# Performance work log

Measured on AMD Instinct MI355X. Metric: run time of the kernel, lower is better.

## Reference

```python
import jax, jax.numpy as jnp
import numpy as np

N_NODES = 100000


def _graph_conv_right(feat, src, dst, W, b, n_nodes):
    # DGL GraphConv(norm='right'): since in_feats > out_feats, apply weight first,
    # then sum-aggregate messages over edges, divide by in-degree (clamped >= 1),
    # add bias, then relu activation.
    h = feat @ W                                   # [N, out]
    msg = jnp.take(h, src, axis=0)                 # [E, out] gather from source nodes
    agg = jax.ops.segment_sum(msg, dst, num_segments=n_nodes)  # [N, out]
    deg = jax.ops.segment_sum(jnp.ones_like(dst, dtype=feat.dtype), dst,
                              num_segments=n_nodes)
    deg = jnp.clip(deg, 1.0, None)                 # allow_zero_in_degree
    out = agg / deg[:, None] + b
    return jax.nn.relu(out)


def setup_inputs() -> dict:
    key = jax.random.key(0)
    ks = jax.random.split(key, 6)
    n_edges = 3200000
    in_dim, hidden_dim, out_dim = 128, 32, 12
    features = jax.random.normal(ks[0], (N_NODES, in_dim), dtype=jnp.float32)
    src = jax.random.randint(ks[1], (n_edges,), 0, N_NODES, dtype=jnp.int64 if jax.config.jax_enable_x64 else jnp.int32)
    dst = jax.random.randint(ks[2], (n_edges,), 0, N_NODES, dtype=jnp.int64 if jax.config.jax_enable_x64 else jnp.int32)
    W1 = jax.random.normal(ks[3], (in_dim, hidden_dim), dtype=jnp.float32) * (1.0 / np.sqrt(in_dim))
    b1 = jnp.zeros((hidden_dim,), dtype=jnp.float32)
    W2 = jax.random.normal(ks[4], (hidden_dim, out_dim), dtype=jnp.float32) * (1.0 / np.sqrt(hidden_dim))
    b2 = jnp.zeros((out_dim,), dtype=jnp.float32)
    return {"features": features, "src": src, "dst": dst,
            "W1": W1, "b1": b1, "W2": W2, "b2": b2}


def reference(features, src, dst, W1, b1, W2, b2):
    x = _graph_conv_right(features, src, dst, W1, b1, N_NODES)
    x = jax.nn.relu(x)  # extra F.relu after layer1 (idempotent, kept for fidelity)
    x = _graph_conv_right(x, src, dst, W2, b2, N_NODES)
    return x
```

## Files before the change

kernel.cpp:

```cpp
#include <hip/hip_runtime.h>
#include <hip/hip_fp16.h>

#define N_IN   128
#define HID    32
#define ODIM   12
#define H2P    16
#define RNODES 128
#define NBMAX  800
#define NBK2   1024
#define BCAP   4608
#define CHUNK  8192

__global__ __launch_bounds__(256) void gemm1_kernel(const float* __restrict__ feat,
                                                    const float* __restrict__ W1,
                                                    __half* __restrict__ h1,
                                                    int* __restrict__ bcur, int nNodes) {
    if (blockIdx.x == 0) {
        ((int4*)bcur)[threadIdx.x] = make_int4(0, 0, 0, 0);
    }
    __shared__ float sF[64 * 132];
    __shared__ float sW[N_IN * HID];
    const int tid = threadIdx.x;
    const int nb  = blockIdx.x * 64;

    {
        const float4* Wv  = (const float4*)W1;
        float4*       sWv = (float4*)sW;
        #pragma unroll
        for (int i = 0; i < 4; ++i) sWv[tid + 256 * i] = Wv[tid + 256 * i];
    }
    #pragma unroll
    for (int i = 0; i < 8; ++i) {
        int f   = tid + 256 * i;
        int row = f >> 5;
        int c4  = f & 31;
        int n   = nb + row;
        float4 v = make_float4(0.f, 0.f, 0.f, 0.f);
        if (n < nNodes) v = *(const float4*)(feat + (size_t)n * N_IN + c4 * 4);
        *(float4*)(sF + row * 132 + c4 * 4) = v;
    }
    __syncthreads();

    const int og = tid & 7;
    const int ng = tid >> 3;
    const int o0 = og * 4;
    const float* f0 = sF + ng * 132;
    const float* f1 = sF + (ng + 32) * 132;

    float acc0[4] = {0.f, 0.f, 0.f, 0.f};
    float acc1[4] = {0.f, 0.f, 0.f, 0.f};
    #pragma unroll 8
    for (int k = 0; k < N_IN; k += 4) {
        float4 a0 = *(const float4*)(f0 + k);
        float4 a1 = *(const float4*)(f1 + k);
        const float a0v[4] = {a0.x, a0.y, a0.z, a0.w};
        const float a1v[4] = {a1.x, a1.y, a1.z, a1.w};
        #pragma unroll
        for (int j = 0; j < 4; ++j) {
            float4 w = *(const float4*)(sW + (k + j) * HID + o0);
            acc0[0] += a0v[j] * w.x; acc0[1] += a0v[j] * w.y;
            acc0[2] += a0v[j] * w.z; acc0[3] += a0v[j] * w.w;
            acc1[0] += a1v[j] * w.x; acc1[1] += a1v[j] * w.y;
            acc1[2] += a1v[j] * w.z; acc1[3] += a1v[j] * w.w;
        }
    }
    int n0 = nb + ng, n1 = nb + ng + 32;
    if (n0 < nNodes) {
        union { __half2 h[2]; float2 f; } u;
        u.h[0] = __floats2half2_rn(acc0[0], acc0[1]);
        u.h[1] = __floats2half2_rn(acc0[2], acc0[3]);
        *(float2*)(h1 + (size_t)n0 * HID + o0) = u.f;
    }
    if (n1 < nNodes) {
        union { __half2 h[2]; float2 f; } u;
        u.h[0] = __floats2half2_rn(acc1[0], acc1[1]);
        u.h[1] = __floats2half2_rn(acc1[2], acc1[3]);
        *(float2*)(h1 + (size_t)n1 * HID + o0) = u.f;
    }
}

__global__ __launch_bounds__(512) void bplace_kernel(const int* __restrict__ src,
                                                     const int* __restrict__ dst,
                                                     int* __restrict__ bcur,
                                                     int* __restrict__ pairs, int nEdges) {
    __shared__ int      lh[NBK2];
    __shared__ int      lcur[NBK2];
    __shared__ int      gofs[NBK2];
    __shared__ int      sAux[512];
    __shared__ int      lst[CHUNK];
    __shared__ unsigned short lbk[CHUNK];

    const int tid  = threadIdx.x;
    const int base = blockIdx.x * CHUNK;
    const int m    = min(CHUNK, nEdges - base);

    lh[tid] = 0; lh[tid + 512] = 0;
    __syncthreads();

    int4 dv[4], sv[4];
    bool ok[4];
    #pragma unroll
    for (int k = 0; k < 4; ++k) {
        int e = base + k * 2048 + tid * 4;
        ok[k] = (e < nEdges);
        if (ok[k]) {
            dv[k] = *(const int4*)(dst + e);
            sv[k] = *(const int4*)(src + e);
        }
    }
    #pragma unroll
    for (int k = 0; k < 4; ++k) {
        if (ok[k]) {
            atomicAdd(&lh[dv[k].x >> 7], 1);
            atomicAdd(&lh[dv[k].y >> 7], 1);
            atomicAdd(&lh[dv[k].z >> 7], 1);
            atomicAdd(&lh[dv[k].w >> 7], 1);
        }
    }
    __syncthreads();

    int c0 = lh[2 * tid], c1 = lh[2 * tid + 1];
    int tsum = c0 + c1;
    sAux[tid] = tsum;
    __syncthreads();
    int inc = tsum;
    for (int off = 1; off < 512; off <<= 1) {
        int t = (tid >= off) ? sAux[tid - off] : 0;
        __syncthreads();
        inc += t;
        sAux[tid] = inc;
        __syncthreads();
    }
    int excl = inc - tsum;
    lh[2 * tid]       = excl;
    lh[2 * tid + 1]   = excl + c0;
    lcur[2 * tid]     = excl;
    lcur[2 * tid + 1] = excl + c0;
    gofs[2 * tid]     = (c0 > 0) ? atomicAdd(&bcur[2 * tid], c0) : 0;
    gofs[2 * tid + 1] = (c1 > 0) ? atomicAdd(&bcur[2 * tid + 1], c1) : 0;
    __syncthreads();

    #pragma unroll
    for (int k = 0; k < 4; ++k) {
        if (ok[k]) {
            int b, p;
            b = dv[k].x >> 7; p = atomicAdd(&lcur[b], 1); lst[p] = ((dv[k].x & 127) << 17) | sv[k].x; lbk[p] = (unsigned short)b;
            b = dv[k].y >> 7; p = atomicAdd(&lcur[b], 1); lst[p] = ((dv[k].y & 127) << 17) | sv[k].y; lbk[p] = (unsigned short)b;
            b = dv[k].z >> 7; p = atomicAdd(&lcur[b], 1); lst[p] = ((dv[k].z & 127) << 17) | sv[k].z; lbk[p] = (unsigned short)b;
            b = dv[k].w >> 7; p = atomicAdd(&lcur[b], 1); lst[p] = ((dv[k].w & 127) << 17) | sv[k].w; lbk[p] = (unsigned short)b;
        }
    }
    __syncthreads();

    for (int i = tid; i < m; i += 512) {
        int b = lbk[i];
        int rank = gofs[b] + (i - lh[b]);
        if (rank < BCAP) pairs[(size_t)b * BCAP + rank] = lst[i];
    }
}

__global__ __launch_bounds__(512) void agg1_kernel(const __half* __restrict__ h1,
                                                   const int* __restrict__ bcur,
                                                   int* __restrict__ pairs,
                                                   const float* __restrict__ b1,
                                                   const float* __restrict__ W2,
                                                   __half* __restrict__ h2,
                                                   float* __restrict__ rdeg,
                                                   int* __restrict__ rowstartg,
                                                   int* __restrict__ countg, int nNodes) {
    __shared__ int   sorted[BCAP];
    __shared__ int   hist[RNODES];
    __shared__ int   scn[RNODES];
    __shared__ int   cur[RNODES];
    __shared__ float sW2[HID * ODIM];
    const int tid = threadIdx.x;
    const int bkt = blockIdx.x;
    const int cnt = min(bcur[bkt], BCAP);
    const size_t pb = (size_t)bkt * BCAP;

    if (tid < RNODES) hist[tid] = 0;
    if (tid < 96) ((float4*)sW2)[tid] = ((const float4*)W2)[tid];
    __syncthreads();

    for (int i = tid; i < cnt; i += 512) atomicAdd(&hist[pairs[pb + i] >> 17], 1);
    __syncthreads();

    int v0 = (tid < RNODES) ? hist[tid] : 0;
    if (tid < RNODES) scn[tid] = v0;
    __syncthreads();
    int inc = v0;
    for (int off = 1; off < RNODES; off <<= 1) {
        int t = (tid < RNODES && tid >= off) ? scn[tid - off] : 0;
        __syncthreads();
        if (tid < RNODES) { inc += t; scn[tid] = inc; }
        __syncthreads();
    }
    if (tid < RNODES) { scn[tid] = inc - v0; cur[tid] = inc - v0; }
    __syncthreads();

    for (int i = tid; i < cnt; i += 512) {
        int v = pairs[pb + i];
        int pos = atomicAdd(&cur[v >> 17], 1);
        sorted[pos] = v & 0x1FFFF;
    }
    __syncthreads();

    for (int i = tid; i < cnt; i += 512) pairs[pb + i] = sorted[i];
    if (tid < RNODES) {
        int n = bkt * RNODES + tid;
        if (n < nNodes) {
            rowstartg[n] = (int)pb + scn[tid];
            countg[n]    = hist[tid];
        }
    }

    const int c   = tid & 15;
    const int grp = tid >> 4;
    const __half2* h1v = (const __half2*)h1;
    const int col = (c < ODIM) ? c : 0;

    #pragma unroll
    for (int g = 0; g < 4; ++g) {
        int nl = g * 32 + grp;
        int n  = bkt * RNODES + nl;
        if (n >= nNodes) continue;
        int dcnt = hist[nl];
        int beg  = scn[nl];
        int end  = beg + dcnt;

        float2 s0 = {0.f, 0.f}, s1 = {0.f, 0.f}, s2 = {0.f, 0.f}, s3 = {0.f, 0.f};
        int i = beg;
        for (; i + 8 <= end; i += 8) {
            int e0 = sorted[i],     e1 = sorted[i + 1], e2 = sorted[i + 2], e3 = sorted[i + 3];
            int e4 = sorted[i + 4], e5 = sorted[i + 5], e6 = sorted[i + 6], e7 = sorted[i + 7];
            float2 f0 = __half22float2(h1v[(size_t)e0 * 16 + c]);
            float2 f1 = __half22float2(h1v[(size_t)e1 * 16 + c]);
            float2 f2 = __half22float2(h1v[(size_t)e2 * 16 + c]);
            float2 f3 = __half22float2(h1v[(size_t)e3 * 16 + c]);
            float2 f4 = __half22float2(h1v[(size_t)e4 * 16 + c]);
            float2 f5 = __half22float2(h1v[(size_t)e5 * 16 + c]);
            float2 f6 = __half22float2(h1v[(size_t)e6 * 16 + c]);
            float2 f7 = __half22float2(h1v[(size_t)e7 * 16 + c]);
            s0.x += f0.x; s0.y += f0.y;  s1.x += f1.x; s1.y += f1.y;
            s2.x += f2.x; s2.y += f2.y;  s3.x += f3.x; s3.y += f3.y;
            s0.x += f4.x; s0.y += f4.y;  s1.x += f5.x; s1.y += f5.y;
            s2.x += f6.x; s2.y += f6.y;  s3.x += f7.x; s3.y += f7.y;
        }
        for (; i + 4 <= end; i += 4) {
            int e0 = sorted[i], e1 = sorted[i + 1], e2 = sorted[i + 2], e3 = sorted[i + 3];
            float2 f0 = __half22float2(h1v[(size_t)e0 * 16 + c]);
            float2 f1 = __half22float2(h1v[(size_t)e1 * 16 + c]);
            float2 f2 = __half22float2(h1v[(size_t)e2 * 16 + c]);
            float2 f3 = __half22float2(h1v[(size_t)e3 * 16 + c]);
            s0.x += f0.x; s0.y += f0.y;  s1.x += f1.x; s1.y += f1.y;
            s2.x += f2.x; s2.y += f2.y;  s3.x += f3.x; s3.y += f3.y;
        }
        for (; i < end; ++i) {
            float2 f = __half22float2(h1v[(size_t)sorted[i] * 16 + c]);
            s0.x += f.x; s0.y += f.y;
        }
        float sumx = (s0.x + s1.x) + (s2.x + s3.x);
        float sumy = (s0.y + s1.y) + (s2.y + s3.y);

        float rd = 1.f / (float)(dcnt < 1 ? 1 : dcnt);
        float x0 = sumx * rd + b1[2 * c];
        float x1 = sumy * rd + b1[2 * c + 1];
        x0 = x0 > 0.f ? x0 : 0.f;
        x1 = x1 > 0.f ? x1 : 0.f;

        float acc = 0.f;
        #pragma unroll
        for (int k = 0; k < 16; ++k) {
            float xk0 = __shfl(x0, k, 16);
            float xk1 = __shfl(x1, k, 16);
            acc += xk0 * sW2[(2 * k) * ODIM + col] + xk1 * sW2[(2 * k + 1) * ODIM + col];
        }
        if (c < ODIM) h2[(size_t)n * H2P + c] = __float2half(acc);
        if (c == 0)   rdeg[n] = rd;
    }
}

__global__ __launch_bounds__(256) void agg2_kernel(const __half* __restrict__ h2,
                                                   const int* __restrict__ rowstartg,
                                                   const int* __restrict__ countg,
                                                   const int* __restrict__ eidx,
                                                   const float* __restrict__ rdeg,
                                                   const float* __restrict__ b2,
                                                   float* __restrict__ out, int nNodes) {
    const int tid = threadIdx.x;
    const int n = blockIdx.x * 32 + (tid >> 3);
    const int c = tid & 7;
    if (n >= nNodes) return;

    const int cnt = countg[n];
    const int beg = rowstartg[n];
    const int end = beg + cnt;
    const int cc  = (c < 6) ? c : 0;
    const __half2* h2v = (const __half2*)h2;

    float2 s0 = {0.f, 0.f}, s1 = {0.f, 0.f}, s2 = {0.f, 0.f}, s3 = {0.f, 0.f};
    int i = beg;
    for (; i + 8 <= end; i += 8) {
        int e0 = eidx[i],     e1 = eidx[i + 1], e2 = eidx[i + 2], e3 = eidx[i + 3];
        int e4 = eidx[i + 4], e5 = eidx[i + 5], e6 = eidx[i + 6], e7 = eidx[i + 7];
        float2 f0 = __half22float2(h2v[(size_t)e0 * 8 + cc]);
        float2 f1 = __half22float2(h2v[(size_t)e1 * 8 + cc]);
        float2 f2 = __half22float2(h2v[(size_t)e2 * 8 + cc]);
        float2 f3 = __half22float2(h2v[(size_t)e3 * 8 + cc]);
        float2 f4 = __half22float2(h2v[(size_t)e4 * 8 + cc]);
        float2 f5 = __half22float2(h2v[(size_t)e5 * 8 + cc]);
        float2 f6 = __half22float2(h2v[(size_t)e6 * 8 + cc]);
        float2 f7 = __half22float2(h2v[(size_t)e7 * 8 + cc]);
        s0.x += f0.x; s0.y += f0.y;  s1.x += f1.x; s1.y += f1.y;
        s2.x += f2.x; s2.y += f2.y;  s3.x += f3.x; s3.y += f3.y;
        s0.x += f4.x; s0.y += f4.y;  s1.x += f5.x; s1.y += f5.y;
        s2.x += f6.x; s2.y += f6.y;  s3.x += f7.x; s3.y += f7.y;
    }
    for (; i + 4 <= end; i += 4) {
        int e0 = eidx[i], e1 = eidx[i + 1], e2 = eidx[i + 2], e3 = eidx[i + 3];
        float2 f0 = __half22float2(h2v[(size_t)e0 * 8 + cc]);
        float2 f1 = __half22float2(h2v[(size_t)e1 * 8 + cc]);
        float2 f2 = __half22float2(h2v[(size_t)e2 * 8 + cc]);
        float2 f3 = __half22float2(h2v[(size_t)e3 * 8 + cc]);
        s0.x += f0.x; s0.y += f0.y;  s1.x += f1.x; s1.y += f1.y;
        s2.x += f2.x; s2.y += f2.y;  s3.x += f3.x; s3.y += f3.y;
    }
    for (; i < end; ++i) {
        float2 f = __half22float2(h2v[(size_t)eidx[i] * 8 + cc]);
        s0.x += f.x; s0.y += f.y;
    }
    float sumx = (s0.x + s1.x) + (s2.x + s3.x);
    float sumy = (s0.y + s1.y) + (s2.y + s3.y);

    float rd = rdeg[n];
    float w0 = sumx * rd + b2[2 * cc];
    float w1 = sumy * rd + b2[2 * cc + 1];
    w0 = w0 > 0.f ? w0 : 0.f;
    w1 = w1 > 0.f ? w1 : 0.f;
    if (c < 6) *(float2*)(out + (size_t)n * ODIM + 2 * c) = make_float2(w0, w1);
}

extern "C" void kernel_launch(void* const* d_in, const int* in_sizes, int n_in,
                              void* d_out, int out_size, void* d_ws, size_t ws_size,
                              hipStream_t stream) {
    const float* feat = (const float*)d_in[0];
    const int*   src  = (const int*)d_in[1];
    const int*   dst  = (const int*)d_in[2];
    const float* W1   = (const float*)d_in[3];
    const float* b1   = (const float*)d_in[4];
    const float* W2   = (const float*)d_in[5];
    const float* b2   = (const float*)d_in[6];
    float* out = (float*)d_out;

    const int nEdges = in_sizes[1];
    const int nNodes = in_sizes[0] / N_IN;
    const int nb     = (nNodes + RNODES - 1) / RNODES;

    __half* h1       = (__half*)d_ws;
    __half* h2       = h1 + (size_t)nNodes * HID;
    float*  rdeg     = (float*)(h2 + (size_t)nNodes * H2P);
    int*    rowstart = (int*)(rdeg + nNodes);
    int*    countg   = rowstart + nNodes;
    int*    bcur     = countg + nNodes;
    int*    pairs    = bcur + NBK2;

    gemm1_kernel<<<(nNodes + 63) / 64, 256, 0, stream>>>(feat, W1, h1, bcur, nNodes);
    bplace_kernel<<<(nEdges + CHUNK - 1) / CHUNK, 512, 0, stream>>>(src, dst, bcur, pairs, nEdges);
    agg1_kernel<<<nb, 512, 0, stream>>>(h1, bcur, pairs, b1, W2, h2, rdeg, rowstart, countg, nNodes);
    agg2_kernel<<<(nNodes + 31) / 32, 256, 0, stream>>>(h2, rowstart, countg, pairs, rdeg, b2, out, nNodes);
}
```

Before: 218.4 us.

## Merge GEMM1 and edge bucket placement into one heterogeneous prep kernel

Combines the node-feature GEMM and the edge bucketing kernel into a single launch whose blocks branch by index: the first blocks bucket edges and the rest compute h1, sharing LDS through a union. The two independent stages can then run concurrently on the GPU, and one kernel launch gap disappears. The bucket-counter reset moves from inside the GEMM kernel to a separate memset. The GEMM blocks now use 512 threads with one row each, and every block reserves the larger bucketing LDS footprint, which can lower occupancy for the GEMM part.

```diff
diff --git a/kernel.cpp b/kernel.cpp
--- a/kernel.cpp
+++ b/kernel.cpp
@@ -11,151 +11,143 @@
 #define BCAP   4608
 #define CHUNK  8192
 
-__global__ __launch_bounds__(256) void gemm1_kernel(const float* __restrict__ feat,
-                                                    const float* __restrict__ W1,
-                                                    __half* __restrict__ h1,
-                                                    int* __restrict__ bcur, int nNodes) {
-    if (blockIdx.x == 0) {
-        ((int4*)bcur)[threadIdx.x] = make_int4(0, 0, 0, 0);
-    }
-    __shared__ float sF[64 * 132];
-    __shared__ float sW[N_IN * HID];
+__global__ __launch_bounds__(512) void prep_kernel(const float* __restrict__ feat,
+                                                   const float* __restrict__ W1,
+                                                   __half* __restrict__ h1,
+                                                   const int* __restrict__ src,
+                                                   const int* __restrict__ dst,
+                                                   int* __restrict__ bcur,
+                                                   int* __restrict__ pairs,
+                                                   int nEdges, int nNodes, int nbPlace) {
+    __shared__ union {
+        struct {
+            int lh[NBK2];
+            int lcur[NBK2];
+            int gofs[NBK2];
+            int sAux[512];
+            int lst[CHUNK];
+            unsigned short lbk[CHUNK];
+        } bp;
+        struct {
+            float sF[64 * 132];
+            float sW[N_IN * HID];
+        } gm;
+    } sm;
+
     const int tid = threadIdx.x;
-    const int nb  = blockIdx.x * 64;
-
-    {
-        const float4* Wv  = (const float4*)W1;
-        float4*       sWv = (float4*)sW;
-        #pragma unroll
-        for (int i = 0; i < 4; ++i) sWv[tid + 256 * i] = Wv[tid + 256 * i];
-    }
-    #pragma unroll
-    for (int i = 0; i < 8; ++i) {
-        int f   = tid + 256 * i;
-        int row = f >> 5;
-        int c4  = f & 31;
-        int n   = nb + row;
-        float4 v = make_float4(0.f, 0.f, 0.f, 0.f);
-        if (n < nNodes) v = *(const float4*)(feat + (size_t)n * N_IN + c4 * 4);
-        *(float4*)(sF + row * 132 + c4 * 4) = v;
-    }
-    __syncthreads();
-
-    const int og = tid & 7;
-    const int ng = tid >> 3;
-    const int o0 = og * 4;
-    const float* f0 = sF + ng * 132;
-    const float* f1 = sF + (ng + 32) * 132;
-
-    float acc0[4] = {0.f, 0.f, 0.f, 0.f};
-    float acc1[4] = {0.f, 0.f, 0.f, 0.f};
-    #pragma unroll 8
-    for (int k = 0; k < N_IN; k += 4) {
-        float4 a0 = *(const float4*)(f0 + k);
-        float4 a1 = *(const float4*)(f1 + k);
-        const float a0v[4] = {a0.x, a0.y, a0.z, a0.w};
-        const float a1v[4] = {a1.x, a1.y, a1.z, a1.w};
-        #pragma unroll
-        for (int j = 0; j < 4; ++j) {
-            float4 w = *(const float4*)(sW + (k + j) * HID + o0);
-            acc0[0] += a0v[j] * w.x; acc0[1] += a0v[j] * w.y;
-            acc0[2] += a0v[j] * w.z; acc0[3] += a0v[j] * w.w;
-            acc1[0] += a1v[j] * w.x; acc1[1] += a1v[j] * w.y;
-            acc1[2] += a1v[j] * w.z; acc1[3] += a1v[j] * w.w;
-        }
-    }
-    int n0 = nb + ng, n1 = nb + ng + 32;
-    if (n0 < nNodes) {
-        union { __half2 h[2]; float2 f; } u;
-        u.h[0] = __floats2half2_rn(acc0[0], acc0[1]);
-        u.h[1] = __floats2half2_rn(acc0[2], acc0[3]);
-        *(float2*)(h1 + (size_t)n0 * HID + o0) = u.f;
-    }
-    if (n1 < nNodes) {
-        union { __half2 h[2]; float2 f; } u;
-        u.h[0] = __floats2half2_rn(acc1[0], acc1[1]);
-        u.h[1] = __floats2half2_rn(acc1[2], acc1[3]);
-        *(float2*)(h1 + (size_t)n1 * HID + o0) = u.f;
-    }
-}
-
-__global__ __launch_bounds__(512) void bplace_kernel(const int* __restrict__ src,
-                                                     const int* __restrict__ dst,
-                                                     int* __restrict__ bcur,
-                                                     int* __restrict__ pairs, int nEdges) {
-    __shared__ int      lh[NBK2];
-    __shared__ int      lcur[NBK2];
-    __shared__ int      gofs[NBK2];
-    __shared__ int      sAux[512];
-    __shared__ int      lst[CHUNK];
-    __shared__ unsigned short lbk[CHUNK];
-
-    const int tid  = threadIdx.x;
-    const int base = blockIdx.x * CHUNK;
-    const int m    = min(CHUNK, nEdges - base);
-
-    lh[tid] = 0; lh[tid + 512] = 0;
-    __syncthreads();
-
-    int4 dv[4], sv[4];
-    bool ok[4];
-    #pragma unroll
-    for (int k = 0; k < 4; ++k) {
-        int e = base + k * 2048 + tid * 4;
-        ok[k] = (e < nEdges);
-        if (ok[k]) {
-            dv[k] = *(const int4*)(dst + e);
-            sv[k] = *(const int4*)(src + e);
-        }
-    }
-    #pragma unroll
-    for (int k = 0; k < 4; ++k) {
-        if (ok[k]) {
-            atomicAdd(&lh[dv[k].x >> 7], 1);
-            atomicAdd(&lh[dv[k].y >> 7], 1);
-            atomicAdd(&lh[dv[k].z >> 7], 1);
-            atomicAdd(&lh[dv[k].w >> 7], 1);
-        }
-    }
-    __syncthreads();
-
-    int c0 = lh[2 * tid], c1 = lh[2 * tid + 1];
-    int tsum = c0 + c1;
-    sAux[tid] = tsum;
-    __syncthreads();
-    int inc = tsum;
-    for (int off = 1; off < 512; off <<= 1) {
-        int t = (tid >= off) ? sAux[tid - off] : 0;
-        __syncthreads();
-        inc += t;
-        sAux[tid] = inc;
-        __syncthreads();
-    }
-    int excl = inc - tsum;
-    lh[2 * tid]       = excl;
-    lh[2 * tid + 1]   = excl + c0;
-    lcur[2 * tid]     = excl;
-    lcur[2 * tid + 1] = excl + c0;
-    gofs[2 * tid]     = (c0 > 0) ? atomicAdd(&bcur[2 * tid], c0) : 0;
-    gofs[2 * tid + 1] = (c1 > 0) ? atomicAdd(&bcur[2 * tid + 1], c1) : 0;
-    __syncthreads();
-
-    #pragma unroll
-    for (int k = 0; k < 4; ++k) {
-        if (ok[k]) {
-            int b, p;
-            b = dv[k].x >> 7; p = atomicAdd(&lcur[b], 1); lst[p] = ((dv[k].x & 127) << 17) | sv[k].x; lbk[p] = (unsigned short)b;
-            b = dv[k].y >> 7; p = atomicAdd(&lcur[b], 1); lst[p] = ((dv[k].y & 127) << 17) | sv[k].y; lbk[p] = (unsigned short)b;
-            b = dv[k].z >> 7; p = atomicAdd(&lcur[b], 1); lst[p] = ((dv[k].z & 127) << 17) | sv[k].z; lbk[p] = (unsigned short)b;
-            b = dv[k].w >> 7; p = atomicAdd(&lcur[b], 1); lst[p] = ((dv[k].w & 127) << 17) | sv[k].w; lbk[p] = (unsigned short)b;
-        }
-    }
-    __syncthreads();
-
-    for (int i = tid; i < m; i += 512) {
-        int b = lbk[i];
-        int rank = gofs[b] + (i - lh[b]);
-        if (rank < BCAP) pairs[(size_t)b * BCAP + rank] = lst[i];
+
+    if (blockIdx.x < nbPlace) {
+        const int base = blockIdx.x * CHUNK;
+        const int m    = min(CHUNK, nEdges - base);
+
+        sm.bp.lh[tid] = 0; sm.bp.lh[tid + 512] = 0;
+        __syncthreads();
+
+        int4 dv[4], sv[4];
+        bool ok[4];
+        #pragma unroll
+        for (int k = 0; k < 4; ++k) {
+            int e = base + k * 2048 + tid * 4;
+            ok[k] = (e < nEdges);
+            if (ok[k]) {
+                dv[k] = *(const int4*)(dst + e);
+                sv[k] = *(const int4*)(src + e);
+            }
+        }
+        #pragma unroll
+        for (int k = 0; k < 4; ++k) {
+            if (ok[k]) {
+                atomicAdd(&sm.bp.lh[dv[k].x >> 7], 1);
+                atomicAdd(&sm.bp.lh[dv[k].y >> 7], 1);
+                atomicAdd(&sm.bp.lh[dv[k].z >> 7], 1);
+                atomicAdd(&sm.bp.lh[dv[k].w >> 7], 1);
+            }
+        }
+        __syncthreads();
+
+        int c0 = sm.bp.lh[2 * tid], c1 = sm.bp.lh[2 * tid + 1];
+        int tsum = c0 + c1;
+        sm.bp.sAux[tid] = tsum;
+        __syncthreads();
+        int inc = tsum;
+        for (int off = 1; off < 512; off <<= 1) {
+            int t = (tid >= off) ? sm.bp.sAux[tid - off] : 0;
+            __syncthreads();
+            inc += t;
+            sm.bp.sAux[tid] = inc;
+            __syncthreads();
+        }
+        int excl = inc - tsum;
+        sm.bp.lh[2 * tid]       = excl;
+        sm.bp.lh[2 * tid + 1]   = excl + c0;
+        sm.bp.lcur[2 * tid]     = excl;
+        sm.bp.lcur[2 * tid + 1] = excl + c0;
+        sm.bp.gofs[2 * tid]     = (c0 > 0) ? atomicAdd(&bcur[2 * tid], c0) : 0;
+        sm.bp.gofs[2 * tid + 1] = (c1 > 0) ? atomicAdd(&bcur[2 * tid + 1], c1) : 0;
+        __syncthreads();
+
+        #pragma unroll
+        for (int k = 0; k < 4; ++k) {
+            if (ok[k]) {
+                int b, p;
+                b = dv[k].x >> 7; p = atomicAdd(&sm.bp.lcur[b], 1); sm.bp.lst[p] = ((dv[k].x & 127) << 17) | sv[k].x; sm.bp.lbk[p] = (unsigned short)b;
+                b = dv[k].y >> 7; p = atomicAdd(&sm.bp.lcur[b], 1); sm.bp.lst[p] = ((dv[k].y & 127) << 17) | sv[k].y; sm.bp.lbk[p] = (unsigned short)b;
+                b = dv[k].z >> 7; p = atomicAdd(&sm.bp.lcur[b], 1); sm.bp.lst[p] = ((dv[k].z & 127) << 17) | sv[k].z; sm.bp.lbk[p] = (unsigned short)b;
+                b = dv[k].w >> 7; p = atomicAdd(&sm.bp.lcur[b], 1); sm.bp.lst[p] = ((dv[k].w & 127) << 17) | sv[k].w; sm.bp.lbk[p] = (unsigned short)b;
+            }
+        }
+        __syncthreads();
+
+        for (int i = tid; i < m; i += 512) {
+            int b = sm.bp.lbk[i];
+            int rank = sm.bp.gofs[b] + (i - sm.bp.lh[b]);
+            if (rank < BCAP) pairs[(size_t)b * BCAP + rank] = sm.bp.lst[i];
+        }
+    } else {
+        const int nb = (blockIdx.x - nbPlace) * 64;
+
+        {
+            const float4* Wv  = (const float4*)W1;
+            float4*       sWv = (float4*)sm.gm.sW;
+            sWv[tid]       = Wv[tid];
+            sWv[tid + 512] = Wv[tid + 512];
+        }
+        #pragma unroll
+        for (int i = 0; i < 4; ++i) {
+            int f   = tid + 512 * i;
+            int row = f >> 5;
+            int c4  = f & 31;
+            int n   = nb + row;
+            float4 v = make_float4(0.f, 0.f, 0.f, 0.f);
+            if (n < nNodes) v = *(const float4*)(feat + (size_t)n * N_IN + c4 * 4);
+            *(float4*)(sm.gm.sF + row * 132 + c4 * 4) = v;
+        }
+        __syncthreads();
+
+        const int og = tid & 7;
+        const int ng = tid >> 3;
+        const int o0 = og * 4;
+        const float* f0 = sm.gm.sF + ng * 132;
+
+        float acc0[4] = {0.f, 0.f, 0.f, 0.f};
+        #pragma unroll 8
+        for (int k = 0; k < N_IN; k += 4) {
+            float4 a0 = *(const float4*)(f0 + k);
+            const float a0v[4] = {a0.x, a0.y, a0.z, a0.w};
+            #pragma unroll
+            for (int j = 0; j < 4; ++j) {
+                float4 w = *(const float4*)(sm.gm.sW + (k + j) * HID + o0);
+                acc0[0] += a0v[j] * w.x; acc0[1] += a0v[j] * w.y;
+                acc0[2] += a0v[j] * w.z; acc0[3] += a0v[j] * w.w;
+            }
+        }
+        int n0 = nb + ng;
+        if (n0 < nNodes) {
+            union { __half2 h[2]; float2 f; } u;
+            u.h[0] = __floats2half2_rn(acc0[0], acc0[1]);
+            u.h[1] = __floats2half2_rn(acc0[2], acc0[3]);
+            *(float2*)(h1 + (size_t)n0 * HID + o0) = u.f;
+        }
     }
 }
 
@@ -355,6 +347,8 @@
     const int nEdges = in_sizes[1];
     const int nNodes = in_sizes[0] / N_IN;
     const int nb     = (nNodes + RNODES - 1) / RNODES;
+    const int nbPlace = (nEdges + CHUNK - 1) / CHUNK;
+    const int nbGemm  = (nNodes + 63) / 64;
 
     __half* h1       = (__half*)d_ws;
     __half* h2       = h1 + (size_t)nNodes * HID;
@@ -364,8 +358,10 @@
     int*    bcur     = countg + nNodes;
     int*    pairs    = bcur + NBK2;
 
-    gemm1_kernel<<<(nNodes + 63) / 64, 256, 0, stream>>>(feat, W1, h1, bcur, nNodes);
-    bplace_kernel<<<(nEdges + CHUNK - 1) / CHUNK, 512, 0, stream>>>(src, dst, bcur, pairs, nEdges);
+    hipMemsetAsync(bcur, 0, NBK2 * sizeof(int), stream);
+
+    prep_kernel<<<nbPlace + nbGemm, 512, 0, stream>>>(feat, W1, h1, src, dst,
+                                                      bcur, pairs, nEdges, nNodes, nbPlace);
     agg1_kernel<<<nb, 512, 0, stream>>>(h1, bcur, pairs, b1, W2, h2, rdeg, rowstart, countg, nNodes);
     agg2_kernel<<<(nNodes + 31) / 32, 256, 0, stream>>>(h2, rowstart, countg, pairs, rdeg, b2, out, nNodes);
 }
```

New measurement: 223.4 us. 2.3% more time.
